# Kernel tuning notes

Measured on AMD Instinct MI355X. Metric: run time of the kernel, lower is better.

## Reference

```python
import jax, jax.numpy as jnp
import numpy as np

VOCAB = 4096
EMBED = 64
NUM_TOKENS = 16
OBS_DIM = 128
HID = 512


def setup_inputs() -> dict:
    key = jax.random.key(0)
    ks = jax.random.split(key, 10)
    s = lambda fan_in: 1.0 / np.sqrt(fan_in)
    inp = {
        "obs": jax.random.normal(ks[0], (1024, 4, OBS_DIM), dtype=jnp.float32),
        "enc_w1": jax.random.normal(ks[1], (OBS_DIM, HID), dtype=jnp.float32) * s(OBS_DIM),
        "enc_b1": jnp.zeros((HID,), dtype=jnp.float32),
        "enc_w2": jax.random.normal(ks[2], (HID, NUM_TOKENS * EMBED), dtype=jnp.float32) * s(HID),
        "enc_b2": jnp.zeros((NUM_TOKENS * EMBED,), dtype=jnp.float32),
        "dec_w1": jax.random.normal(ks[3], (NUM_TOKENS * EMBED, HID), dtype=jnp.float32) * s(NUM_TOKENS * EMBED),
        "dec_b1": jnp.zeros((HID,), dtype=jnp.float32),
        "dec_w2": jax.random.normal(ks[4], (HID, OBS_DIM), dtype=jnp.float32) * s(HID),
        "dec_b2": jnp.zeros((OBS_DIM,), dtype=jnp.float32),
        # nn.Embedding init: uniform(-1/vocab, 1/vocab)
        "codebook": jax.random.uniform(ks[5], (VOCAB, EMBED), dtype=jnp.float32,
                                        minval=-1.0 / VOCAB, maxval=1.0 / VOCAB),
    }
    return inp


def reference(obs, enc_w1, enc_b1, enc_w2, enc_b2, dec_w1, dec_b1, dec_w2, dec_b2, codebook):
    shape = obs.shape  # (B, N, obs_dim)
    x = obs.reshape(-1, shape[-1])  # (BN, obs_dim)
    # encoder MLP
    h = jax.nn.relu(x @ enc_w1 + enc_b1)
    z = (h @ enc_w2 + enc_b2).reshape(-1, NUM_TOKENS, EMBED)  # (BN, n, e)
    b = z.shape[0]
    zf = z.reshape(-1, EMBED)  # (BN*n, e)
    # ||z||^2 + ||c||^2 - 2 z.c  -> (BN*n, vocab)
    dist = (jnp.sum(zf * zf, axis=1, keepdims=True)
            + jnp.sum(codebook * codebook, axis=1)
            - 2.0 * zf @ codebook.T)
    tokens = jnp.argmin(dist, axis=-1)  # (BN*n,)
    z_q = codebook[tokens].reshape(b, NUM_TOKENS, EMBED)
    # straight-through
    dec_in = z + jax.lax.stop_gradient(z_q - z)
    d = dec_in.reshape(b, NUM_TOKENS * EMBED)
    rec = jax.nn.relu(d @ dec_w1 + dec_b1) @ dec_w2 + dec_b2  # (BN, obs_dim)
    z_out = z.reshape(*shape[:-1], NUM_TOKENS, EMBED)
    zq_out = z_q.reshape(*shape[:-1], NUM_TOKENS, EMBED)
    rec_out = rec.reshape(*shape[:-1], OBS_DIM)
    return z_out, zq_out, rec_out
```

## Files before the change

### kernel.cpp

```cpp
#include <hip/hip_runtime.h>
#include <math.h>

#define VOCAB 4096
#define EMBED 64
#define OBSD  128
#define HIDD  512
#define BNR   4096
#define ZR    65536
#define ZD    1024
#define NCHUNK 4
#define CHSZ  (VOCAB / NCHUNK)
#define TCODES 64
#define NTILES (CHSZ / TCODES)

#define MARGIN_SCALED 4.0e-3f

#define SSTR 136
#define GSTR (8 * SSTR)
#define TYPSZ (4 * GSTR)

#define RB 8

typedef _Float16 half8  __attribute__((ext_vector_type(8)));
typedef _Float16 half4  __attribute__((ext_vector_type(4)));
typedef short    bf16x8 __attribute__((ext_vector_type(8)));
typedef float    f32x4  __attribute__((ext_vector_type(4)));

__device__ __forceinline__ f32x4 mfma_f16(half8 a, half8 b, f32x4 c){
  return __builtin_amdgcn_mfma_f32_16x16x32_f16(a,b,c,0,0,0);
}
__device__ __forceinline__ f32x4 mfma_bf(bf16x8 a, bf16x8 b, f32x4 c){
  return __builtin_amdgcn_mfma_f32_16x16x32_bf16(a,b,c,0,0,0);
}
__device__ __forceinline__ unsigned short f2bf(float f){
  union{float f; unsigned u;} x; x.f=f;
  unsigned u = x.u + 0x7fffu + ((x.u>>16)&1u);
  return (unsigned short)(u>>16);
}
__device__ __forceinline__ float bf2f(unsigned short h){
  union{unsigned u; float f;} x; x.u = ((unsigned)h)<<16; return x.f;
}
__device__ __forceinline__ void split3(float w, unsigned short& b1,
                                       unsigned short& b2, unsigned short& b3){
  b1 = f2bf(w); float r  = w - bf2f(b1);
  b2 = f2bf(r); float r2 = r - bf2f(b2);
  b3 = f2bf(r2);
}
__device__ __forceinline__ bf16x8 ldbf(const unsigned short* p){
  return *(const bf16x8*)(const void*)p;
}

__global__ __launch_bounds__(256) void prep_all_kernel(
    const float* __restrict__ cb, _Float16* __restrict__ chi,
    float* __restrict__ bcol, double* __restrict__ bcold,
    float* __restrict__ cbT,
    const float* __restrict__ ew1, unsigned short* __restrict__ w1t1,
    unsigned short* __restrict__ w1t2, unsigned short* __restrict__ w1t3,
    const float* __restrict__ ew2, unsigned short* __restrict__ w2t1,
    unsigned short* __restrict__ w2t2, unsigned short* __restrict__ w2t3,
    const float* __restrict__ obs, unsigned short* __restrict__ o1,
    unsigned short* __restrict__ o2, unsigned short* __restrict__ o3,
    const float* __restrict__ dw1, unsigned short* __restrict__ d1t,
    const float* __restrict__ dw2, unsigned short* __restrict__ d2t,
    int* __restrict__ rcnt)
{
  const int b = blockIdx.x;
  const int t = threadIdx.x;
  if (b == 0 && t == 0) *rcnt = 0;
  if (b < 16) {
    int j = b * 256 + t;
    double s = 0.0;
    #pragma unroll 8
    for (int d = 0; d < EMBED; ++d) {
      float c = cb[j * EMBED + d];
      s += (double)c * (double)c;
      chi[j * EMBED + d] = (_Float16)(c * 4096.0f);
      cbT[(size_t)d * VOCAB + j] = c;
    }
    double bd = -0.5 * s * 4096.0;
    bcold[j] = bd;
    bcol[j] = (float)bd;
  } else if (b < 272) {
    int e = (b - 16) * 256 + t;
    int n = e / OBSD, k = e % OBSD;
    split3(ew1[(size_t)k * HIDD + n], w1t1[e], w1t2[e], w1t3[e]);
  } else if (b < 2320) {
    int e = (b - 272) * 256 + t;
    int n = e / HIDD, k = e % HIDD;
    split3(ew2[(size_t)k * ZD + n], w2t1[e], w2t2[e], w2t3[e]);
  } else if (b < 4368) {
    int e = (b - 2320) * 256 + t;
    split3(obs[e], o1[e], o2[e], o3[e]);
  } else if (b < 6416) {
    int e = (b - 4368) * 256 + t;
    int n = e / ZD, k = e % ZD;
    d1t[e] = f2bf(dw1[(size_t)k * HIDD + n]);
  } else {
    int e = (b - 6416) * 256 + t;
    int n = e / HIDD, k = e % HIDD;
    d2t[e] = f2bf(dw2[(size_t)k * OBSD + n]);
  }
}

template<int NSPLIT, int MS, bool RELU, int OUT>
__global__ __launch_bounds__(512) void gemm_lds_kernel(
    const unsigned short* __restrict__ A1, const unsigned short* __restrict__ A2,
    const unsigned short* __restrict__ A3,
    const unsigned short* __restrict__ B1, const unsigned short* __restrict__ B2,
    const unsigned short* __restrict__ B3,
    const float* __restrict__ bias, int M, int N, int K,
    unsigned short* __restrict__ H1, unsigned short* __restrict__ H2,
    unsigned short* __restrict__ H3,
    float* __restrict__ Z, _Float16* __restrict__ Zhi, _Float16* __restrict__ Zlo)
{
  constexpr int BM  = MS * 32;
  constexpr int ASZ = BM * 40;
  constexpr int BSZ = 128 * 40;
  constexpr int ACH = BM * 4;
  constexpr int TCH = ACH + 512;
  __shared__ unsigned short lds[NSPLIT * (ASZ + BSZ)];

  const int tid  = threadIdx.x;
  const int wave = tid >> 6;
  const int lane = tid & 63;
  const int l15  = lane & 15;
  const int lg   = lane >> 4;
  const int wm   = wave >> 2;
  const int wn   = wave & 3;
  const int m0   = blockIdx.x * BM;
  const int n0   = blockIdx.y * 128;

  const unsigned short* Aps[3] = {A1, A2, A3};
  const unsigned short* Bps[3] = {B1, B2, B3};

  size_t goff[2]; int lb[2], pst[2]; bool valid[2], isA[2];
  #pragma unroll
  for (int sl = 0; sl < 2; ++sl) {
    int c = tid + sl * 512;
    valid[sl] = c < TCH;
    bool a = c < ACH;
    isA[sl] = a;
    int cr = a ? c : (c - ACH);
    if (!valid[sl]) cr = 0;
    int row = cr >> 2, o16 = cr & 3;
    goff[sl] = (size_t)(a ? m0 + row : n0 + row) * K + o16 * 8;
    lb[sl]   = (a ? 0 : NSPLIT * ASZ) + row * 40 + o16 * 8;
    pst[sl]  = a ? ASZ : BSZ;
  }

  #pragma unroll
  for (int sl = 0; sl < 2; ++sl) if (valid[sl]) {
    #pragma unroll
    for (int p = 0; p < NSPLIT; ++p)
      *(bf16x8*)(void*)&lds[lb[sl] + p * pst[sl]] =
          ldbf((isA[sl] ? Aps[p] : Bps[p]) + goff[sl]);
  }
  __syncthreads();

  double accd[MS][2][4];
  f32x4  accf[MS][2];
  #pragma unroll
  for (int ms = 0; ms < MS; ++ms)
    #pragma unroll
    for (int ns = 0; ns < 2; ++ns) {
      accf[ms][ns] = (f32x4){0.f, 0.f, 0.f, 0.f};
      #pragma unroll
      for (int r = 0; r < 4; ++r) accd[ms][ns][r] = 0.0;
    }

  const int KS = K / 32;
  for (int step = 0; step < KS; ++step) {
    bf16x8 nv[NSPLIT][2];
    const bool pre = (step + 1 < KS);
    if (pre) {
      #pragma unroll
      for (int sl = 0; sl < 2; ++sl) if (valid[sl]) {
        #pragma unroll
        for (int p = 0; p < NSPLIT; ++p)
          nv[p][sl] = ldbf((isA[sl] ? Aps[p] : Bps[p]) + goff[sl]
                           + (size_t)(step + 1) * 32);
      }
    }

    bf16x8 af[NSPLIT][MS], bfr[NSPLIT][2];
    #pragma unroll
    for (int ms = 0; ms < MS; ++ms) {
      const int ar = (wm * MS * 16 + ms * 16 + l15) * 40 + lg * 8;
      #pragma unroll
      for (int p = 0; p < NSPLIT; ++p)
        af[p][ms] = *(const bf16x8*)(const void*)&lds[p * ASZ + ar];
    }
    #pragma unroll
    for (int ns = 0; ns < 2; ++ns) {
      const int br = (wn * 32 + ns * 16 + l15) * 40 + lg * 8;
      #pragma unroll
      for (int p = 0; p < NSPLIT; ++p)
        bfr[p][ns] = *(const bf16x8*)(const void*)&lds[NSPLIT * ASZ + p * BSZ + br];
    }

    #pragma unroll
    for (int ms = 0; ms < MS; ++ms)
      #pragma unroll
      for (int ns = 0; ns < 2; ++ns) {
        if constexpr (NSPLIT == 3) {
          f32x4 acc = {0.f, 0.f, 0.f, 0.f};
          acc = mfma_bf(af[0][ms], bfr[2][ns], acc);
          acc = mfma_bf(af[1][ms], bfr[1][ns], acc);
          acc = mfma_bf(af[2][ms], bfr[0][ns], acc);
          acc = mfma_bf(af[0][ms], bfr[1][ns], acc);
          acc = mfma_bf(af[1][ms], bfr[0][ns], acc);
          acc = mfma_bf(af[0][ms], bfr[0][ns], acc);
          #pragma unroll
          for (int r = 0; r < 4; ++r) accd[ms][ns][r] += (double)acc[r];
        } else {
          accf[ms][ns] = mfma_bf(af[0][ms], bfr[0][ns], accf[ms][ns]);
        }
      }

    __syncthreads();
    if (pre) {
      #pragma unroll
      for (int sl = 0; sl < 2; ++sl) if (valid[sl]) {
        #pragma unroll
        for (int p = 0; p < NSPLIT; ++p)
          *(bf16x8*)(void*)&lds[lb[sl] + p * pst[sl]] = nv[p][sl];
      }
    }
    __syncthreads();
  }

  #pragma unroll
  for (int ms = 0; ms < MS; ++ms)
    #pragma unroll
    for (int ns = 0; ns < 2; ++ns)
      #pragma unroll
      for (int r = 0; r < 4; ++r) {
        int row = m0 + wm * MS * 16 + ms * 16 + lg * 4 + r;
        int col = n0 + wn * 32 + ns * 16 + l15;
        float v = (NSPLIT == 3 ? (float)accd[ms][ns][r] : accf[ms][ns][r])
                  + bias[col];
        if constexpr (RELU) v = v > 0.f ? v : 0.f;
        size_t o = (size_t)row * N + col;
        if constexpr (OUT == 0) {
          split3(v, H1[o], H2[o], H3[o]);
        } else if constexpr (OUT == 1) {
          Z[o] = v;
          _Float16 hi = (_Float16)v;
          Zhi[o] = hi;
          Zlo[o] = (_Float16)(v - (float)hi);
        } else {
          H1[o] = f2bf(v);
        }
      }
}

template<bool RELU, bool OUTBF>
__global__ __launch_bounds__(256) void dec_mfma_kernel(
    const unsigned short* __restrict__ A, const unsigned short* __restrict__ B,
    const float* __restrict__ bias, int M, int N, int K,
    unsigned short* __restrict__ Obf, float* __restrict__ Of)
{
  const int tid  = threadIdx.x;
  const int wave = tid >> 6;
  const int lane = tid & 63;
  const int l15  = lane & 15;
  const int lg   = lane >> 4;
  const int m0 = blockIdx.x * 64 + (wave >> 1) * 32;
  const int n0 = blockIdx.y * 64 + (wave & 1) * 32;

  f32x4 acc[2][2] = {};
  for (int k0 = 0; k0 < K; k0 += 32) {
    bf16x8 a[2], b[2];
    #pragma unroll
    for (int ms = 0; ms < 2; ++ms)
      a[ms] = ldbf(A + (size_t)(m0 + ms * 16 + l15) * K + k0 + lg * 8);
    #pragma unroll
    for (int ns = 0; ns < 2; ++ns)
      b[ns] = ldbf(B + (size_t)(n0 + ns * 16 + l15) * K + k0 + lg * 8);
    #pragma unroll
    for (int ms = 0; ms < 2; ++ms)
      #pragma unroll
      for (int ns = 0; ns < 2; ++ns)
        acc[ms][ns] = mfma_bf(a[ms], b[ns], acc[ms][ns]);
  }
  #pragma unroll
  for (int ms = 0; ms < 2; ++ms)
    #pragma unroll
    for (int ns = 0; ns < 2; ++ns)
      #pragma unroll
      for (int r = 0; r < 4; ++r) {
        int row = m0 + ms * 16 + lg * 4 + r;
        int col = n0 + ns * 16 + l15;
        float v = acc[ms][ns][r] + bias[col];
        if constexpr (RELU) v = v > 0.f ? v : 0.f;
        if constexpr (OUTBF) Obf[(size_t)row * N + col] = f2bf(v);
        else                 Of[(size_t)row * N + col] = v;
      }
}

__global__ __launch_bounds__(1024) void dist_kernel(
    const _Float16* __restrict__ zhi, const _Float16* __restrict__ zlo,
    const _Float16* __restrict__ chi, const float* __restrict__ bcol,
    float2* __restrict__ pb2, int* __restrict__ pidx)
{
  __shared__ _Float16 sh[2][TYPSZ];
  __shared__ float    sbc[CHSZ];

  const int tid  = threadIdx.x;
  const int wave = tid >> 6;
  const int lane = tid & 63;
  const int l15  = lane & 15;
  const int lg   = lane >> 4;
  const int rowW = blockIdx.x * 512 + wave * 32;
  const int ch   = blockIdx.y;

  half8 ah0[2], ah1[2], al0[2], al1[2];
  #pragma unroll
  for (int s = 0; s < 2; ++s) {
    const size_t base = (size_t)(rowW + s * 16 + l15) * EMBED + lg * 8;
    ah0[s] = *(const half8*)(zhi + base);
    ah1[s] = *(const half8*)(zhi + base + 32);
    al0[s] = *(const half8*)(zlo + base);
    al1[s] = *(const half8*)(zlo + base + 32);
  }

  const _Float16* gsrc = chi + (size_t)ch * CHSZ * EMBED;
  const int code = tid >> 4, rem = tid & 15, sl = rem >> 1, hf = rem & 1;
  const int ld = (code >> 4) * GSTR + sl * SSTR + (code & 15) * 8 + hf * 4;
  const size_t goff = (size_t)code * EMBED + sl * 8 + hf * 4;

  sbc[tid] = bcol[ch * CHSZ + tid];

  *(half4*)(&sh[0][ld]) = *(const half4*)(gsrc + goff);
  __syncthreads();

  float best[2][4], second[2][4];
  int   bidx[2][4];
  #pragma unroll
  for (int s = 0; s < 2; ++s)
    #pragma unroll
    for (int r = 0; r < 4; ++r) {
      best[s][r] = -INFINITY; second[s][r] = -INFINITY; bidx[s][r] = 0;
    }

  for (int tile = 0; tile < NTILES; ++tile) {
    const int buf = tile & 1;
    half4 v0 = {};
    if (tile + 1 < NTILES)
      v0 = *(const half4*)(gsrc + (size_t)(tile + 1) * (TCODES * EMBED) + goff);

    const _Float16* ph = &sh[buf][0];
    #pragma unroll
    for (int grp = 0; grp < 4; ++grp) {
      const int rb = grp * GSTR + l15 * 8;
      half8 bh0 = *(const half8*)(ph + rb + lg * SSTR);
      half8 bh1 = *(const half8*)(ph + rb + (4 + lg) * SSTR);
      const int cloc = tile * TCODES + grp * 16 + l15;
      const int col  = ch * CHSZ + cloc;
      const float vb = sbc[cloc];
      const f32x4 seed = {vb, vb, vb, vb};
      #pragma unroll
      for (int s = 0; s < 2; ++s) {
        f32x4 acc = seed;
        acc = mfma_f16(al0[s], bh0, acc);
        acc = mfma_f16(al1[s], bh1, acc);
        acc = mfma_f16(ah0[s], bh0, acc);
        acc = mfma_f16(ah1[s], bh1, acc);
        #pragma unroll
        for (int r = 0; r < 4; ++r) {
          float v = acc[r];
          float sn = __builtin_amdgcn_fmed3f(second[s][r], best[s][r], v);
          bool gt = v > best[s][r];
          best[s][r] = gt ? v : best[s][r];
          bidx[s][r] = gt ? col : bidx[s][r];
          second[s][r] = sn;
        }
      }
    }
    if (tile + 1 < NTILES)
      *(half4*)(&sh[buf ^ 1][ld]) = v0;
    __syncthreads();
  }

  #pragma unroll
  for (int m = 1; m <= 8; m <<= 1) {
    #pragma unroll
    for (int s = 0; s < 2; ++s)
      #pragma unroll
      for (int r = 0; r < 4; ++r) {
        float ob = __shfl_xor(best[s][r], m, 64);
        float os = __shfl_xor(second[s][r], m, 64);
        int   oi = __shfl_xor(bidx[s][r], m, 64);
        float mn = fminf(best[s][r], ob);
        second[s][r] = fmaxf(mn, fmaxf(second[s][r], os));
        if (ob > best[s][r]) { best[s][r] = ob; bidx[s][r] = oi; }
      }
  }

  if (l15 == 0) {
    #pragma unroll
    for (int s = 0; s < 2; ++s)
      #pragma unroll
      for (int r = 0; r < 4; ++r) {
        int row = rowW + s * 16 + lg * 4 + r;
        pb2 [(size_t)ch * ZR + row] = make_float2(best[s][r], second[s][r]);
        pidx[(size_t)ch * ZR + row] = bidx[s][r];
      }
  }
}

__global__ __launch_bounds__(256) void merge_kernel(
    const float2* __restrict__ pb2, const int* __restrict__ pidx,
    int* __restrict__ tokens, int* __restrict__ rcnt, int* __restrict__ rrows)
{
  int r = blockIdx.x * 256 + threadIdx.x;
  float b = -INFINITY, s = -INFINITY;
  int bi = 0;
  #pragma unroll
  for (int c = 0; c < NCHUNK; ++c) {
    float2 p = pb2[(size_t)c * ZR + r];
    int    i = pidx[(size_t)c * ZR + r];
    if (p.x > b) { s = fmaxf(b, p.y); b = p.x; bi = i; }
    else         { s = fmaxf(s, p.x); }
  }
  tokens[r] = bi;
  if (b - s < MARGIN_SCALED) {
    int p = atomicAdd(rcnt, 1);
    if (p < ZR) rrows[p] = r;
  }
}

__global__ __launch_bounds__(512) void rescue_kernel(
    const int* __restrict__ cnt, const int* __restrict__ rows,
    const float* __restrict__ z, const float* __restrict__ cbT,
    const double* __restrict__ bcold, int* __restrict__ tokens)
{
  __shared__ double zl[RB][EMBED];
  __shared__ int    ridx[RB];
  __shared__ double swv[8][RB];
  __shared__ int    swi[8][RB];

  int n = *cnt; if (n > ZR) n = ZR;
  int nb = (n + RB - 1) / RB;
  const int tid = threadIdx.x;

  for (int batch = blockIdx.x; batch < nb; batch += gridDim.x) {
    __syncthreads();
    if (tid < RB) {
      int e = batch * RB + tid;
      ridx[tid] = (e < n) ? rows[e] : -1;
    }
    __syncthreads();
    {
      int r = tid >> 6, k = tid & 63;
      int rr = ridx[r];
      zl[r][k] = (rr >= 0) ? (double)z[(size_t)rr * EMBED + k] : 0.0;
    }
    __syncthreads();

    double best[RB]; int bidx[RB];
    #pragma unroll
    for (int r = 0; r < RB; ++r) { best[r] = -1.0e300; bidx[r] = 0; }

    for (int c = 0; c < VOCAB / 512; ++c) {
      const int j = c * 512 + tid;
      double acc[RB] = {};
      #pragma unroll 16
      for (int k = 0; k < EMBED; ++k) {
        double cd = (double)cbT[(size_t)k * VOCAB + j];
        #pragma unroll
        for (int r = 0; r < RB; ++r)
          acc[r] = fma(cd, zl[r][k], acc[r]);
      }
      const double bc = bcold[j];
      #pragma unroll
      for (int r = 0; r < RB; ++r) {
        double s = 4096.0 * acc[r] + bc;
        if (s > best[r]) { best[r] = s; bidx[r] = j; }
      }
    }

    #pragma unroll
    for (int m = 1; m < 64; m <<= 1) {
      #pragma unroll
      for (int r = 0; r < RB; ++r) {
        double ov = __shfl_xor(best[r], m, 64);
        int    oi = __shfl_xor(bidx[r], m, 64);
        if (ov > best[r] || (ov == best[r] && oi < bidx[r])) {
          best[r] = ov; bidx[r] = oi;
        }
      }
    }
    const int wv = tid >> 6, ln = tid & 63;
    if (ln == 0)
      #pragma unroll
      for (int r = 0; r < RB; ++r) { swv[wv][r] = best[r]; swi[wv][r] = bidx[r]; }
    __syncthreads();
    if (tid < RB) {
      int r = tid;
      double bv = swv[0][r]; int bi = swi[0][r];
      #pragma unroll
      for (int w2 = 1; w2 < 8; ++w2) {
        double ov = swv[w2][r]; int oi = swi[w2][r];
        if (ov > bv || (ov == bv && oi < bi)) { bv = ov; bi = oi; }
      }
      if (ridx[r] >= 0) tokens[ridx[r]] = bi;
    }
  }
}

__global__ __launch_bounds__(256) void gather_kernel(
    const int* __restrict__ tokens, const float* __restrict__ cb,
    float* __restrict__ zq, unsigned short* __restrict__ zqb)
{
  int g = blockIdx.x * 256 + threadIdx.x;
  int row = g >> 4;
  int part = g & 15;
  int tok = tokens[row];
  float4 cv = ((const float4*)cb)[tok * 16 + part];
  ((float4*)zq)[g] = cv;
  ushort4 o;
  o.x = f2bf(cv.x); o.y = f2bf(cv.y); o.z = f2bf(cv.z); o.w = f2bf(cv.w);
  ((ushort4*)zqb)[g] = o;
}

extern "C" void kernel_launch(void* const* d_in, const int* in_sizes, int n_in,
                              void* d_out, int out_size, void* d_ws, size_t ws_size,
                              hipStream_t stream)
{
  const float* obs = (const float*)d_in[0];
  const float* ew1 = (const float*)d_in[1];
  const float* eb1 = (const float*)d_in[2];
  const float* ew2 = (const float*)d_in[3];
  const float* eb2 = (const float*)d_in[4];
  const float* dw1 = (const float*)d_in[5];
  const float* db1 = (const float*)d_in[6];
  const float* dw2 = (const float*)d_in[7];
  const float* db2 = (const float*)d_in[8];
  const float* cb  = (const float*)d_in[9];

  float* out_z   = (float*)d_out;
  float* out_zq  = out_z + (size_t)ZR * EMBED;
  float* out_rec = out_z + 2 * (size_t)ZR * EMBED;

  unsigned short* h1 = (unsigned short*)out_zq;
  unsigned short* h2 = h1 + (size_t)BNR * HIDD;
  unsigned short* h3 = h2 + (size_t)BNR * HIDD;

  char* w = (char*)d_ws;
  _Float16* chi  = (_Float16*)w; w += (size_t)VOCAB * EMBED * 2;
  float*    bcol = (float*)w;    w += 64 * 1024;
  double*   bcold = (double*)w;  w += 64 * 1024;
  float*    cbT  = (float*)w;    w += (size_t)VOCAB * EMBED * 4;
  _Float16* zhi  = (_Float16*)w; w += (size_t)ZR * EMBED * 2;
  _Float16* zlo  = (_Float16*)w; w += (size_t)ZR * EMBED * 2;
  unsigned short* w1t1 = (unsigned short*)w; w += (size_t)HIDD * OBSD * 2;
  unsigned short* w1t2 = (unsigned short*)w; w += (size_t)HIDD * OBSD * 2;
  unsigned short* w1t3 = (unsigned short*)w; w += (size_t)HIDD * OBSD * 2;
  unsigned short* w2t1 = (unsigned short*)w; w += (size_t)ZD * HIDD * 2;
  unsigned short* w2t2 = (unsigned short*)w; w += (size_t)ZD * HIDD * 2;
  unsigned short* w2t3 = (unsigned short*)w; w += (size_t)ZD * HIDD * 2;
  unsigned short* d1t  = (unsigned short*)w; w += (size_t)HIDD * ZD * 2;
  unsigned short* d2t  = (unsigned short*)w; w += (size_t)OBSD * HIDD * 2;
  int* tokens = (int*)w;  w += (size_t)ZR * 4;
  int* rrows  = (int*)w;  w += (size_t)ZR * 4;
  int* rcnt   = (int*)w;  w += 64;
  float2* pb2 = (float2*)w; w += (size_t)NCHUNK * ZR * 8;
  int*   pidx = (int*)w;    w += (size_t)NCHUNK * ZR * 4;

  unsigned short* o1 = (unsigned short*)zhi;
  unsigned short* o2 = o1 + (size_t)BNR * OBSD;
  unsigned short* o3 = o2 + (size_t)BNR * OBSD;
  unsigned short* zqb  = (unsigned short*)zhi;
  unsigned short* hdec = (unsigned short*)zlo;

  prep_all_kernel<<<6672, 256, 0, stream>>>(
      cb, chi, bcol, bcold, cbT,
      ew1, w1t1, w1t2, w1t3,
      ew2, w2t1, w2t2, w2t3,
      obs, o1, o2, o3,
      dw1, d1t, dw2, d2t, rcnt);

  gemm_lds_kernel<3, 1, true, 0><<<dim3(BNR / 32, HIDD / 128), 512, 0, stream>>>(
      o1, o2, o3, w1t1, w1t2, w1t3, eb1, BNR, HIDD, OBSD,
      h1, h2, h3, nullptr, nullptr, nullptr);
  gemm_lds_kernel<3, 2, false, 1><<<dim3(BNR / 64, ZD / 128), 512, 0, stream>>>(
      h1, h2, h3, w2t1, w2t2, w2t3, eb2, BNR, ZD, HIDD,
      nullptr, nullptr, nullptr, out_z, zhi, zlo);

  dist_kernel<<<dim3(ZR / 512, NCHUNK), 1024, 0, stream>>>(
      zhi, zlo, chi, bcol, pb2, pidx);
  merge_kernel<<<ZR / 256, 256, 0, stream>>>(pb2, pidx, tokens, rcnt, rrows);
  rescue_kernel<<<512, 512, 0, stream>>>(rcnt, rrows, out_z, cbT, bcold, tokens);
  gather_kernel<<<(ZR * 16) / 256, 256, 0, stream>>>(tokens, cb, out_zq, zqb);

  gemm_lds_kernel<1, 1, true, 2><<<dim3(BNR / 32, HIDD / 128), 512, 0, stream>>>(
      zqb, zqb, zqb, d1t, d1t, d1t, db1, BNR, HIDD, ZD,
      hdec, nullptr, nullptr, nullptr, nullptr, nullptr);
  dec_mfma_kernel<false, false><<<dim3(BNR / 64, OBSD / 64), 256, 0, stream>>>(
      hdec, d2t, db2, BNR, OBSD, HIDD, nullptr, out_rec);
}
```

Measured before the change: 222.3 us.

## Drop low-half z term from distance MFMAs and widen rescue margin

The distance kernel now uses only the fp16 high part of z, which halves the MFMA work and removes the zlo loads and writes. To cover the extra rounding error, the near-tie margin that sends rows to the exact rescue path is doubled. Separately, the weight-transpose prep loops now read coalesced and scatter their writes. The risks are that more rows fall into the rescue kernel, and that the scattered writes in prep may cost more than the coalesced reads save.

```diff
diff --git a/kernel.cpp b/kernel.cpp
--- a/kernel.cpp
+++ b/kernel.cpp
@@ -13,7 +13,7 @@
 #define TCODES 64
 #define NTILES (CHSZ / TCODES)
 
-#define MARGIN_SCALED 4.0e-3f
+#define MARGIN_SCALED 8.0e-3f
 
 #define SSTR 136
 #define GSTR (8 * SSTR)
@@ -82,23 +82,23 @@
     bcol[j] = (float)bd;
   } else if (b < 272) {
     int e = (b - 16) * 256 + t;
-    int n = e / OBSD, k = e % OBSD;
-    split3(ew1[(size_t)k * HIDD + n], w1t1[e], w1t2[e], w1t3[e]);
+    int k = e / HIDD, n = e % HIDD;
+    split3(ew1[e], w1t1[n * OBSD + k], w1t2[n * OBSD + k], w1t3[n * OBSD + k]);
   } else if (b < 2320) {
     int e = (b - 272) * 256 + t;
-    int n = e / HIDD, k = e % HIDD;
-    split3(ew2[(size_t)k * ZD + n], w2t1[e], w2t2[e], w2t3[e]);
+    int k = e / ZD, n = e % ZD;
+    split3(ew2[e], w2t1[n * HIDD + k], w2t2[n * HIDD + k], w2t3[n * HIDD + k]);
   } else if (b < 4368) {
     int e = (b - 2320) * 256 + t;
     split3(obs[e], o1[e], o2[e], o3[e]);
   } else if (b < 6416) {
     int e = (b - 4368) * 256 + t;
-    int n = e / ZD, k = e % ZD;
-    d1t[e] = f2bf(dw1[(size_t)k * HIDD + n]);
+    int k = e / HIDD, n = e % HIDD;
+    d1t[(size_t)n * ZD + k] = f2bf(dw1[e]);
   } else {
     int e = (b - 6416) * 256 + t;
-    int n = e / HIDD, k = e % HIDD;
-    d2t[e] = f2bf(dw2[(size_t)k * OBSD + n]);
+    int k = e / OBSD, n = e % OBSD;
+    d2t[(size_t)n * HIDD + k] = f2bf(dw2[e]);
   }
 }
 
@@ -111,7 +111,7 @@
     const float* __restrict__ bias, int M, int N, int K,
     unsigned short* __restrict__ H1, unsigned short* __restrict__ H2,
     unsigned short* __restrict__ H3,
-    float* __restrict__ Z, _Float16* __restrict__ Zhi, _Float16* __restrict__ Zlo)
+    float* __restrict__ Z, _Float16* __restrict__ Zhi)
 {
   constexpr int BM  = MS * 32;
   constexpr int ASZ = BM * 40;
@@ -245,9 +245,7 @@
           split3(v, H1[o], H2[o], H3[o]);
         } else if constexpr (OUT == 1) {
           Z[o] = v;
-          _Float16 hi = (_Float16)v;
-          Zhi[o] = hi;
-          Zlo[o] = (_Float16)(v - (float)hi);
+          Zhi[o] = (_Float16)v;
         } else {
           H1[o] = f2bf(v);
         }
@@ -299,8 +297,8 @@
 }
 
 __global__ __launch_bounds__(1024) void dist_kernel(
-    const _Float16* __restrict__ zhi, const _Float16* __restrict__ zlo,
-    const _Float16* __restrict__ chi, const float* __restrict__ bcol,
+    const _Float16* __restrict__ zhi, const _Float16* __restrict__ chi,
+    const float* __restrict__ bcol,
     float2* __restrict__ pb2, int* __restrict__ pidx)
 {
   __shared__ _Float16 sh[2][TYPSZ];
@@ -314,14 +312,12 @@
   const int rowW = blockIdx.x * 512 + wave * 32;
   const int ch   = blockIdx.y;
 
-  half8 ah0[2], ah1[2], al0[2], al1[2];
+  half8 ah0[2], ah1[2];
   #pragma unroll
   for (int s = 0; s < 2; ++s) {
     const size_t base = (size_t)(rowW + s * 16 + l15) * EMBED + lg * 8;
     ah0[s] = *(const half8*)(zhi + base);
     ah1[s] = *(const half8*)(zhi + base + 32);
-    al0[s] = *(const half8*)(zlo + base);
-    al1[s] = *(const half8*)(zlo + base + 32);
   }
 
   const _Float16* gsrc = chi + (size_t)ch * CHSZ * EMBED;
@@ -362,8 +358,6 @@
       #pragma unroll
       for (int s = 0; s < 2; ++s) {
         f32x4 acc = seed;
-        acc = mfma_f16(al0[s], bh0, acc);
-        acc = mfma_f16(al1[s], bh1, acc);
         acc = mfma_f16(ah0[s], bh0, acc);
         acc = mfma_f16(ah1[s], bh1, acc);
         #pragma unroll
@@ -553,7 +547,7 @@
   double*   bcold = (double*)w;  w += 64 * 1024;
   float*    cbT  = (float*)w;    w += (size_t)VOCAB * EMBED * 4;
   _Float16* zhi  = (_Float16*)w; w += (size_t)ZR * EMBED * 2;
-  _Float16* zlo  = (_Float16*)w; w += (size_t)ZR * EMBED * 2;
+  char*     spare = w;           w += (size_t)ZR * EMBED * 2;
   unsigned short* w1t1 = (unsigned short*)w; w += (size_t)HIDD * OBSD * 2;
   unsigned short* w1t2 = (unsigned short*)w; w += (size_t)HIDD * OBSD * 2;
   unsigned short* w1t3 = (unsigned short*)w; w += (size_t)HIDD * OBSD * 2;
@@ -572,7 +566,7 @@
   unsigned short* o2 = o1 + (size_t)BNR * OBSD;
   unsigned short* o3 = o2 + (size_t)BNR * OBSD;
   unsigned short* zqb  = (unsigned short*)zhi;
-  unsigned short* hdec = (unsigned short*)zlo;
+  unsigned short* hdec = (unsigned short*)spare;
 
   prep_all_kernel<<<6672, 256, 0, stream>>>(
       cb, chi, bcol, bcold, cbT,
@@ -583,20 +577,20 @@
 
   gemm_lds_kernel<3, 1, true, 0><<<dim3(BNR / 32, HIDD / 128), 512, 0, stream>>>(
       o1, o2, o3, w1t1, w1t2, w1t3, eb1, BNR, HIDD, OBSD,
-      h1, h2, h3, nullptr, nullptr, nullptr);
+      h1, h2, h3, nullptr, nullptr);
   gemm_lds_kernel<3, 2, false, 1><<<dim3(BNR / 64, ZD / 128), 512, 0, stream>>>(
       h1, h2, h3, w2t1, w2t2, w2t3, eb2, BNR, ZD, HIDD,
-      nullptr, nullptr, nullptr, out_z, zhi, zlo);
+      nullptr, nullptr, nullptr, out_z, zhi);
 
   dist_kernel<<<dim3(ZR / 512, NCHUNK), 1024, 0, stream>>>(
-      zhi, zlo, chi, bcol, pb2, pidx);
+      zhi, chi, bcol, pb2, pidx);
   merge_kernel<<<ZR / 256, 256, 0, stream>>>(pb2, pidx, tokens, rcnt, rrows);
   rescue_kernel<<<512, 512, 0, stream>>>(rcnt, rrows, out_z, cbT, bcold, tokens);
   gather_kernel<<<(ZR * 16) / 256, 256, 0, stream>>>(tokens, cb, out_zq, zqb);
 
   gemm_lds_kernel<1, 1, true, 2><<<dim3(BNR / 32, HIDD / 128), 512, 0, stream>>>(
       zqb, zqb, zqb, d1t, d1t, d1t, db1, BNR, HIDD, ZD,
-      hdec, nullptr, nullptr, nullptr, nullptr, nullptr);
+      hdec, nullptr, nullptr, nullptr, nullptr);
   dec_mfma_kernel<false, false><<<dim3(BNR / 64, OBSD / 64), 256, 0, stream>>>(
       hdec, d2t, db2, BNR, OBSD, HIDD, nullptr, out_rec);
 }
```

Measured after the change: 212.9 us. 4.2% less time.
